# Performance work log

Hardware: AMD Instinct MI355X
Metric: run time of the kernel (lower is better)

## Reference

```python
import jax, jax.numpy as jnp
import numpy as np

# Model constants (match init_kwargs)
H = 256          # hidden_dim
NH = 4           # num_heads
L = 4            # gnn_layers
T = 4            # transformer_layers
KMAX = 10        # k_max for overlap embedding
MAXD = 32        # MAX_DIST
INC = 119        # in_channels (atom vocab)
ED = 5           # edge_dim (bond vocab)
B = 64           # graphs per batch
M_SUB = 32       # subgraphs per graph (m)
KNODE = 32       # nodes per subgraph (k)
S = B * M_SUB    # total subgraphs = 2048
N = S * KNODE    # flattened nodes = 65536
E = 131072       # intra-subgraph directed edges


def _ln(x, g, b):
    mu = x.mean(-1, keepdims=True)
    var = ((x - mu) ** 2).mean(-1, keepdims=True)
    return (x - mu) * jax.lax.rsqrt(var + 1e-5) * g + b


def setup_inputs() -> dict:
    key = jax.random.key(0)
    ks = iter(jax.random.split(key, 24))
    nk = lambda: next(ks)
    rn = lambda k_, shp: 0.02 * jax.random.normal(k_, shp, dtype=jnp.float32)

    x_ids = jax.random.randint(nk(), (N,), 0, INC)
    edge_ids = jax.random.randint(nk(), (E,), 0, ED)
    # intra-subgraph edges: endpoints stay within each block of KNODE nodes
    eps_per = E // S
    base = jnp.repeat(jnp.arange(S) * KNODE, eps_per)
    src = base + jax.random.randint(nk(), (E,), 0, KNODE)
    dst = base + jax.random.randint(nk(), (E,), 0, KNODE)
    ns = jax.random.randint(nk(), (S, KNODE), 0, 500)
    padm = jax.random.uniform(nk(), (S, KNODE)) < 0.1
    nodes_sampled = jnp.where(padm, -1, ns)
    dist = jax.random.randint(nk(), (N,), 0, MAXD + 1)
    lp = -5.0 * jax.random.uniform(nk(), (S,))

    return {
        'x_ids': x_ids, 'edge_ids': edge_ids, 'src': src, 'dst': dst,
        'nodes_sampled': nodes_sampled, 'dist': dist, 'lp': lp,
        'atom_emb': rn(nk(), (INC, H)), 'bond_emb': rn(nk(), (ED, H)),
        'dist_emb': rn(nk(), (MAXD + 1, H)),
        'logp_W': rn(nk(), (H,)), 'logp_b': jnp.zeros((H,)),
        'gnn_eps': jnp.zeros((L,)),
        'gnn_W1': rn(nk(), (L, H, H)), 'gnn_b1': jnp.zeros((L, H)),
        'gnn_W2': rn(nk(), (L, H, H)), 'gnn_b2': jnp.zeros((L, H)),
        'ln1_g': jnp.ones((T, H)), 'ln1_b': jnp.zeros((T, H)),
        'qkv_W': rn(nk(), (T, H, 3 * H)),
        'out_W': rn(nk(), (T, H, H)), 'out_b': jnp.zeros((T, H)),
        'ln2_g': jnp.ones((T, H)), 'ln2_b': jnp.zeros((T, H)),
        'f1_W': rn(nk(), (T, H, 4 * H)), 'f1_b': jnp.zeros((T, 4 * H)),
        'f2_W': rn(nk(), (T, 4 * H, H)), 'f2_b': jnp.zeros((T, H)),
        'lnout_g': jnp.ones((H,)), 'lnout_b': jnp.zeros((H,)),
        'overlap_emb': rn(nk(), (KMAX + 1,)),
        'ht_alpha': jnp.ones(()),
    }


def reference(x_ids, edge_ids, src, dst, nodes_sampled, dist, lp,
              atom_emb, bond_emb, dist_emb, logp_W, logp_b,
              gnn_eps, gnn_W1, gnn_b1, gnn_W2, gnn_b2,
              ln1_g, ln1_b, qkv_W, out_W, out_b, ln2_g, ln2_b,
              f1_W, f1_b, f2_W, f2_b, lnout_g, lnout_b,
              overlap_emb, ht_alpha):
    # ---- flatten / embed node features ----
    valid = (nodes_sampled >= 0).reshape(N)
    valid_f = valid.astype(jnp.float32)[:, None]
    lp = jnp.where(jnp.isfinite(lp), lp, 0.0)
    sub_batch = jnp.arange(N) // KNODE
    dist_c = jnp.clip(dist, 0, MAXD)
    logp_pe = jax.nn.relu(lp[sub_batch][:, None] * logp_W + logp_b)
    h = (atom_emb[x_ids] + dist_emb[dist_c] + logp_pe) * valid_f  # [N,H]
    e = bond_emb[edge_ids]                                        # [E,H]

    # ---- GINE message passing ----
    for l in range(L):
        msg = jax.nn.relu(h[src] + e)                       # [E,H] gather
        agg = jax.ops.segment_sum(msg, dst, num_segments=N) # [N,H] scatter-add
        z = (1.0 + gnn_eps[l]) * h + agg
        z = jax.nn.relu(z @ gnn_W1[l] + gnn_b1[l])
        h = (z @ gnn_W2[l] + gnn_b2[l]) * valid_f

    # ---- pool roots into [B, m, H] tokens ----
    root = jnp.arange(S) * KNODE
    x = h[root].reshape(B, M_SUB, H)
    lp2 = lp.reshape(B, M_SUB)

    # ---- pairwise subgraph overlap bias ----
    nodes = nodes_sampled.reshape(B, M_SUB, KNODE)
    vmask = nodes >= 0
    # eq[b,i,j,ki,kj]: node ki of subgraph i equals node kj of subgraph j
    eq = nodes[:, :, None, :, None] == nodes[:, None, :, None, :]
    overlap = (eq.any(-1) & vmask[:, :, None, :]).sum(-1)  # [B,m,m]
    lp_c = jnp.clip(lp2, -30.0, 0.0)
    bias = overlap_emb[jnp.clip(overlap, 0, KMAX)] - ht_alpha * lp_c[:, None, :]
    bias = bias[:, None]  # [B,1,m,m], broadcast over heads

    # ---- relative-bias transformer ----
    hd = H // NH
    scale = 1.0 / np.sqrt(hd).astype(np.float32)
    for t in range(T):
        r = _ln(x, ln1_g[t], ln1_b[t])
        q, k_, v = jnp.split(r @ qkv_W[t], 3, axis=-1)
        q = q.reshape(B, M_SUB, NH, hd)
        k_ = k_.reshape(B, M_SUB, NH, hd)
        v = v.reshape(B, M_SUB, NH, hd)
        scores = jnp.einsum('bihd,bjhd->bhij', q, k_) * scale + bias
        attn = jax.nn.softmax(scores, axis=-1)
        o = jnp.einsum('bhij,bjhd->bihd', attn, v).reshape(B, M_SUB, H)
        x = x + o @ out_W[t] + out_b[t]
        r2 = _ln(x, ln2_g[t], ln2_b[t])
        x = x + jax.nn.gelu(r2 @ f1_W[t] + f1_b[t], approximate=False) @ f2_W[t] + f2_b[t]

    x = _ln(x, lnout_g, lnout_b)
    # HT-weighted mean over subgraph tokens
    w = jax.nn.softmax(-lp_c, axis=1)
    return (w[:, :, None] * x).sum(1)  # [B,H]
```

## Files before the change

kernel.cpp:

```cpp
#include <hip/hip_runtime.h>
#include <hip/hip_bf16.h>
#include <math.h>

#define HDIM   256
#define NHEAD  4
#define LLAY   4
#define TLAY   4
#define KMAXC  10
#define MAXD   32
#define BATCH  64
#define MSUB   32
#define KNODE  32
#define SSUB   2048
#define NNODE  65536
#define NEDGE  131072
#define EPSPER 64
#define EDN    5

typedef unsigned short u16;
typedef __attribute__((ext_vector_type(8))) short bf16x8;
typedef __attribute__((ext_vector_type(4))) float f32x4;

__device__ __forceinline__ float us2f(u16 u) {
    union { unsigned int i; float f; } x; x.i = ((unsigned int)u) << 16; return x.f;
}
__device__ __forceinline__ u16 f2us(float v) {
    union { float f; unsigned int i; } x; x.f = v;
    unsigned int u = x.i;
    u += 0x7fffu + ((u >> 16) & 1u);
    return (u16)(u >> 16);
}
__device__ __forceinline__ float finite_or_zero(float v) {
    return (v == v && fabsf(v) <= 3.0e38f) ? v : 0.0f;
}
__device__ __forceinline__ void gll16(const u16* g, u16* l) {
    __builtin_amdgcn_global_load_lds(
        (const __attribute__((address_space(1))) unsigned int*)g,
        (__attribute__((address_space(3))) unsigned int*)l, 16, 0, 0);
}

__global__ __launch_bounds__(256) void k_csr(
    const int* __restrict__ src, const int* __restrict__ dst,
    const int* __restrict__ eid, u16* __restrict__ perm, u16* __restrict__ off)
{
    __shared__ int sL[4][64], dL[4][64], eL[4][64];
    int wave = threadIdx.x >> 6, lane = threadIdx.x & 63;
    int sgi = blockIdx.x * 4 + wave;
    sL[wave][lane] = src[sgi * 64 + lane] - sgi * KNODE;
    dL[wave][lane] = dst[sgi * 64 + lane] - sgi * KNODE;
    eL[wave][lane] = eid[sgi * 64 + lane];
    __syncthreads();
    if (lane < 32) {
        int cnt = 0;
        for (int e = 0; e < 64; ++e) cnt += (dL[wave][e] == lane) ? 1 : 0;
        int incl = cnt;
        #pragma unroll
        for (int d = 1; d < 32; d <<= 1) {
            int v = __shfl_up(incl, d, 64);
            if (lane >= d) incl += v;
        }
        int start = incl - cnt;
        off[sgi * 32 + lane] = (u16)start;
        int pos = start;
        for (int e = 0; e < 64; ++e) {
            if (dL[wave][e] == lane) {
                perm[sgi * 64 + pos] = (u16)((sL[wave][e] << 3) | eL[wave][e]);
                ++pos;
            }
        }
    }
}

__global__ __launch_bounds__(256) void k_wtrans(
    const float* __restrict__ W, u16* __restrict__ WT, int K, int N)
{
    __shared__ float til[32][33];
    int k0 = blockIdx.x * 32, n0 = blockIdx.y * 32, s = blockIdx.z;
    const float* Wb = W + (size_t)s * K * N;
    u16* Tb = WT + (size_t)s * N * K;
    int j = threadIdx.x & 31, i0 = threadIdx.x >> 5;
    #pragma unroll
    for (int it = 0; it < 4; ++it) {
        int i = i0 + it * 8;
        til[i][j] = Wb[(size_t)(k0 + i) * N + n0 + j];
    }
    __syncthreads();
    #pragma unroll
    for (int it = 0; it < 4; ++it) {
        int i = i0 + it * 8;
        Tb[(size_t)(n0 + i) * K + k0 + j] = f2us(til[j][i]);
    }
}

__global__ __launch_bounds__(256, 3) void k_gnn4(
    const int* __restrict__ x_ids, const int* __restrict__ dist,
    const int* __restrict__ nodes, const float* __restrict__ lp,
    const float* __restrict__ atom_emb, const float* __restrict__ dist_emb,
    const float* __restrict__ logp_W, const float* __restrict__ logp_b,
    const u16* __restrict__ perm, const u16* __restrict__ off,
    const float* __restrict__ bond_emb, const float* __restrict__ eps_arr,
    const float* __restrict__ b1a, const float* __restrict__ b2a,
    const u16* __restrict__ W1T, const u16* __restrict__ W2T,
    float* __restrict__ x)
{
    __shared__ __align__(16) unsigned char smem[38912];
    u16*   hz    = (u16*)smem;
    float* bondL = (float*)(smem + 32768);
    u16*   permL = (u16*)(smem + 32768 + 5120);
    u16*   offL  = (u16*)(smem + 32768 + 5120 + 256);
    float* validL= (float*)(smem + 32768 + 5120 + 512);
    float* epsL  = (float*)(smem + 32768 + 5120 + 512 + 256);

    int tid = threadIdx.x, lane = tid & 63, wave = tid >> 6;
    int row0 = blockIdx.x * 64;
    int fr = lane & 15, quad = lane >> 4;

    for (int i = tid; i < EDN * 256; i += 256) bondL[i] = bond_emb[i];
    if (tid < 128) permL[tid] = perm[blockIdx.x * 128 + tid];
    if (tid < 64) {
        offL[tid] = off[blockIdx.x * 64 + tid];
        validL[tid] = (nodes[row0 + tid] >= 0) ? 1.0f : 0.0f;
    }
    if (tid < 4) epsL[tid] = eps_arr[tid];

    {
        int m = tid & 63, qd = tid >> 6;
        int rg = row0 + m;
        float valid = (nodes[rg] >= 0) ? 1.0f : 0.0f;
        float lpv = finite_or_zero(lp[rg >> 5]);
        int dc = dist[rg]; dc = dc < 0 ? 0 : (dc > MAXD ? MAXD : dc);
        int xid = x_ids[rg];
        #pragma unroll
        for (int k = 0; k < 8; ++k) {
            int cc = qd * 8 + k, c = cc * 8;
            float4 a0 = *reinterpret_cast<const float4*>(atom_emb + xid * 256 + c);
            float4 a1 = *reinterpret_cast<const float4*>(atom_emb + xid * 256 + c + 4);
            float4 d0 = *reinterpret_cast<const float4*>(dist_emb + dc * 256 + c);
            float4 d1 = *reinterpret_cast<const float4*>(dist_emb + dc * 256 + c + 4);
            float4 w0 = *reinterpret_cast<const float4*>(logp_W + c);
            float4 w1 = *reinterpret_cast<const float4*>(logp_W + c + 4);
            float4 p0 = *reinterpret_cast<const float4*>(logp_b + c);
            float4 p1 = *reinterpret_cast<const float4*>(logp_b + c + 4);
            union { bf16x8 v; ushort4 h[2]; } o;
            o.h[0] = (ushort4){
                f2us((a0.x + d0.x + fmaxf(lpv * w0.x + p0.x, 0.f)) * valid),
                f2us((a0.y + d0.y + fmaxf(lpv * w0.y + p0.y, 0.f)) * valid),
                f2us((a0.z + d0.z + fmaxf(lpv * w0.z + p0.z, 0.f)) * valid),
                f2us((a0.w + d0.w + fmaxf(lpv * w0.w + p0.w, 0.f)) * valid) };
            o.h[1] = (ushort4){
                f2us((a1.x + d1.x + fmaxf(lpv * w1.x + p1.x, 0.f)) * valid),
                f2us((a1.y + d1.y + fmaxf(lpv * w1.y + p1.y, 0.f)) * valid),
                f2us((a1.z + d1.z + fmaxf(lpv * w1.z + p1.z, 0.f)) * valid),
                f2us((a1.w + d1.w + fmaxf(lpv * w1.w + p1.w, 0.f)) * valid) };
            *reinterpret_cast<bf16x8*>(hz + m * 256 + ((cc ^ (m & 7)) * 8)) = o.v;
        }
    }
    __syncthreads();

    int rl = tid >> 3, g8 = tid & 7;
    for (int l = 0; l < LLAY; ++l) {
        float ep1 = 1.0f + epsL[l];
        for (int p = 0; p < 2; ++p) {
            int row = p * 32 + rl;
            int e0 = offL[p * 32 + rl];
            int e1 = (rl < 31) ? offL[p * 32 + rl + 1] : 64;
            float a[32];
            #pragma unroll
            for (int q = 0; q < 32; ++q) a[q] = 0.f;
            for (int j = e0; j < e1; ++j) {
                int ent = permL[p * 64 + j];
                int sl = p * 32 + (ent >> 3);
                int be = ent & 7;
                #pragma unroll
                for (int q = 0; q < 4; ++q) {
                    union { bf16x8 v; u16 s[8]; } hv;
                    hv.v = *reinterpret_cast<const bf16x8*>(
                        hz + sl * 256 + (((g8 * 4 + q) ^ (sl & 7)) * 8));
                    const float* bp = bondL + be * 256 + g8 * 32 + q * 8;
                    float4 bo0 = *reinterpret_cast<const float4*>(bp);
                    float4 bo1 = *reinterpret_cast<const float4*>(bp + 4);
                    a[q*8+0] += fmaxf(us2f(hv.s[0]) + bo0.x, 0.f);
                    a[q*8+1] += fmaxf(us2f(hv.s[1]) + bo0.y, 0.f);
                    a[q*8+2] += fmaxf(us2f(hv.s[2]) + bo0.z, 0.f);
                    a[q*8+3] += fmaxf(us2f(hv.s[3]) + bo0.w, 0.f);
                    a[q*8+4] += fmaxf(us2f(hv.s[4]) + bo1.x, 0.f);
                    a[q*8+5] += fmaxf(us2f(hv.s[5]) + bo1.y, 0.f);
                    a[q*8+6] += fmaxf(us2f(hv.s[6]) + bo1.z, 0.f);
                    a[q*8+7] += fmaxf(us2f(hv.s[7]) + bo1.w, 0.f);
                }
            }
            __syncthreads();
            #pragma unroll
            for (int q = 0; q < 4; ++q) {
                u16* ptr = hz + row * 256 + (((g8 * 4 + q) ^ (row & 7)) * 8);
                union { bf16x8 v; u16 s[8]; } hv, ov;
                hv.v = *reinterpret_cast<const bf16x8*>(ptr);
                #pragma unroll
                for (int k = 0; k < 8; ++k)
                    ov.s[k] = f2us(ep1 * us2f(hv.s[k]) + a[q * 8 + k]);
                *reinterpret_cast<bf16x8*>(ptr) = ov.v;
            }
        }
        __syncthreads();

        const u16* W1 = W1T + l * 65536;
        const float* b1 = b1a + l * 256;
        bf16x8 wf[4][8];
        #pragma unroll
        for (int i = 0; i < 4; ++i)
            #pragma unroll
            for (int kc = 0; kc < 8; ++kc)
                wf[i][kc] = *reinterpret_cast<const bf16x8*>(
                    W1 + (size_t)(wave * 64 + i * 16 + fr) * 256 + kc * 32 + quad * 8);
        f32x4 acc[4][4];
        #pragma unroll
        for (int i = 0; i < 4; ++i)
            #pragma unroll
            for (int j = 0; j < 4; ++j) acc[i][j] = (f32x4){0.f, 0.f, 0.f, 0.f};
        #pragma unroll
        for (int kc = 0; kc < 8; ++kc) {
            bf16x8 bfv[4];
            #pragma unroll
            for (int j = 0; j < 4; ++j) {
                int m = j * 16 + fr;
                bfv[j] = *reinterpret_cast<const bf16x8*>(hz + m * 256 + (((kc * 4 + quad) ^ (m & 7)) * 8));
            }
            #pragma unroll
            for (int i = 0; i < 4; ++i)
                #pragma unroll
                for (int j = 0; j < 4; ++j)
                    acc[i][j] = __builtin_amdgcn_mfma_f32_16x16x32_bf16(wf[i][kc], bfv[j], acc[i][j], 0, 0, 0);
        }
        __syncthreads();
        #pragma unroll
        for (int i = 0; i < 4; ++i) {
            int n1b = wave * 64 + i * 16 + quad * 4;
            float4 bb = *reinterpret_cast<const float4*>(b1 + n1b);
            #pragma unroll
            for (int j = 0; j < 4; ++j) {
                int m = j * 16 + fr;
                ushort4 o = { f2us(fmaxf(acc[i][j][0] + bb.x, 0.f)),
                              f2us(fmaxf(acc[i][j][1] + bb.y, 0.f)),
                              f2us(fmaxf(acc[i][j][2] + bb.z, 0.f)),
                              f2us(fmaxf(acc[i][j][3] + bb.w, 0.f)) };
                *reinterpret_cast<ushort4*>(hz + m * 256 + (((n1b >> 3) ^ (m & 7)) * 8) + (n1b & 7)) = o;
            }
        }
        __syncthreads();

        const u16* W2 = W2T + l * 65536;
        const float* b2 = b2a + l * 256;
        #pragma unroll
        for (int i = 0; i < 4; ++i)
            #pragma unroll
            for (int kc = 0; kc < 8; ++kc)
                wf[i][kc] = *reinterpret_cast<const bf16x8*>(
                    W2 + (size_t)(wave * 64 + i * 16 + fr) * 256 + kc * 32 + quad * 8);
        #pragma unroll
        for (int i = 0; i < 4; ++i)
            #pragma unroll
            for (int j = 0; j < 4; ++j) acc[i][j] = (f32x4){0.f, 0.f, 0.f, 0.f};
        #pragma unroll
        for (int kc = 0; kc < 8; ++kc) {
            bf16x8 bfv[4];
            #pragma unroll
            for (int j = 0; j < 4; ++j) {
                int m = j * 16 + fr;
                bfv[j] = *reinterpret_cast<const bf16x8*>(hz + m * 256 + (((kc * 4 + quad) ^ (m & 7)) * 8));
            }
            #pragma unroll
            for (int i = 0; i < 4; ++i)
                #pragma unroll
                for (int j = 0; j < 4; ++j)
                    acc[i][j] = __builtin_amdgcn_mfma_f32_16x16x32_bf16(wf[i][kc], bfv[j], acc[i][j], 0, 0, 0);
        }
        __syncthreads();

        if (l < LLAY - 1) {
            #pragma unroll
            for (int i = 0; i < 4; ++i) {
                int n2b = wave * 64 + i * 16 + quad * 4;
                float4 bb = *reinterpret_cast<const float4*>(b2 + n2b);
                #pragma unroll
                for (int j = 0; j < 4; ++j) {
                    int m = j * 16 + fr;
                    float vm = validL[m];
                    ushort4 o = { f2us((acc[i][j][0] + bb.x) * vm),
                                  f2us((acc[i][j][1] + bb.y) * vm),
                                  f2us((acc[i][j][2] + bb.z) * vm),
                                  f2us((acc[i][j][3] + bb.w) * vm) };
                    *reinterpret_cast<ushort4*>(hz + m * 256 + (((n2b >> 3) ^ (m & 7)) * 8) + (n2b & 7)) = o;
                }
            }
            __syncthreads();
        } else {
            if (fr == 0) {
                #pragma unroll
                for (int i = 0; i < 4; ++i) {
                    int n2b = wave * 64 + i * 16 + quad * 4;
                    float4 bb = *reinterpret_cast<const float4*>(b2 + n2b);
                    #pragma unroll
                    for (int jj = 0; jj < 2; ++jj) {
                        int j = jj * 2, m = j * 16;
                        float vm = validL[m];
                        float4 o = { (acc[i][j][0] + bb.x) * vm,
                                     (acc[i][j][1] + bb.y) * vm,
                                     (acc[i][j][2] + bb.z) * vm,
                                     (acc[i][j][3] + bb.w) * vm };
                        *reinterpret_cast<float4*>(
                            x + (size_t)(blockIdx.x * 2 + (m >> 5)) * 256 + n2b) = o;
                    }
                }
            }
        }
    }
}

__global__ __launch_bounds__(1024) void k_bias(
    const int* __restrict__ nodes, const float* __restrict__ lp,
    const float* __restrict__ ovl_emb, const float* __restrict__ alpha_p,
    float* __restrict__ bias)
{
    int b = blockIdx.x, tid = threadIdx.x;
    __shared__ int nd[32][32];
    __shared__ unsigned int bmv[32][17];
    __shared__ float lpc[32];
    __shared__ float emb[16];
    nd[tid >> 5][tid & 31] = nodes[b * 1024 + tid];
    if (tid < 512) bmv[tid >> 4][tid & 15] = 0u;
    if (tid < 32) {
        float l = finite_or_zero(lp[b * 32 + tid]);
        l = l < -30.f ? -30.f : (l > 0.f ? 0.f : l);
        lpc[tid] = l;
    }
    if (tid >= 64 && tid < 64 + KMAXC + 1) emb[tid - 64] = ovl_emb[tid - 64];
    __syncthreads();
    int own = nd[tid >> 5][tid & 31];
    if (own >= 0) atomicOr(&bmv[tid >> 5][own >> 5], 1u << (own & 31));
    __syncthreads();
    int i = tid >> 5, j = tid & 31;
    float alpha = alpha_p[0];
    int cnt = 0;
    #pragma unroll
    for (int k = 0; k < 32; ++k) {
        int nk = nd[i][k];
        if (nk >= 0) cnt += (int)((bmv[j][nk >> 5] >> (nk & 31)) & 1u);
    }
    bias[b * 1024 + tid] = emb[cnt > KMAXC ? KMAXC : cnt] - alpha * lpc[j];
}

__global__ __launch_bounds__(256) void k_gemmA_ln(
    const float* __restrict__ X, const u16* __restrict__ BT,
    const float* __restrict__ ln_g, const float* __restrict__ ln_b,
    const float* __restrict__ bias, u16* __restrict__ C,
    int N, int act)
{
    __shared__ __align__(16) u16 As[64 * 256];
    __shared__ __align__(16) u16 Bs[2][64 * 32];
    int tid = threadIdx.x, lane = tid & 63, wave = tid >> 6;
    int wm = wave >> 1, wn = wave & 1;
    int bm = blockIdx.y * 64, bn = blockIdx.x * 64;
    int fr = lane & 15, quad = lane >> 4;

    const u16* gB = BT + (size_t)(bn + wave * 16 + (lane >> 2)) * 256 + (lane & 3) * 8;
    gll16(gB, &Bs[0][wave * 512]);

    #pragma unroll
    for (int rr = 0; rr < 16; ++rr) {
        int r = wave * 16 + rr;
        float4 xv = *reinterpret_cast<const float4*>(X + (size_t)(bm + r) * 256 + lane * 4);
        float s = xv.x + xv.y + xv.z + xv.w;
        #pragma unroll
        for (int o2 = 32; o2 > 0; o2 >>= 1) s += __shfl_xor(s, o2);
        float mu = s * (1.0f / 256.0f);
        float d0 = xv.x - mu, d1 = xv.y - mu, d2 = xv.z - mu, d3 = xv.w - mu;
        float sq = d0 * d0 + d1 * d1 + d2 * d2 + d3 * d3;
        #pragma unroll
        for (int o2 = 32; o2 > 0; o2 >>= 1) sq += __shfl_xor(sq, o2);
        float rs = rsqrtf(sq * (1.0f / 256.0f) + 1e-5f);
        int c = lane * 4;
        float4 gv = *reinterpret_cast<const float4*>(ln_g + c);
        float4 bv = *reinterpret_cast<const float4*>(ln_b + c);
        ushort4 o = { f2us(d0 * rs * gv.x + bv.x), f2us(d1 * rs * gv.y + bv.y),
                      f2us(d2 * rs * gv.z + bv.z), f2us(d3 * rs * gv.w + bv.w) };
        *reinterpret_cast<ushort4*>(As + r * 256 + (((lane >> 1) ^ (r & 7)) * 8) + (lane & 1) * 4) = o;
    }
    __syncthreads();

    f32x4 acc[2][2];
    #pragma unroll
    for (int i = 0; i < 2; ++i)
        #pragma unroll
        for (int j = 0; j < 2; ++j) acc[i][j] = (f32x4){0.f, 0.f, 0.f, 0.f};
    for (int kc = 0; kc < 8; ++kc) {
        int buf = kc & 1;
        if (kc < 7) gll16(gB + (kc + 1) * 32, &Bs[buf ^ 1][wave * 512]);
        bf16x8 af[2], bfr[2];
        #pragma unroll
        for (int i = 0; i < 2; ++i) {
            int m = wm * 32 + i * 16 + fr;
            af[i] = *reinterpret_cast<const bf16x8*>(As + m * 256 + (((kc * 4 + quad) ^ (m & 7)) * 8));
        }
        #pragma unroll
        for (int j = 0; j < 2; ++j)
            bfr[j] = *reinterpret_cast<const bf16x8*>(&Bs[buf][(wn * 32 + j * 16 + fr) * 32 + quad * 8]);
        #pragma unroll
        for (int i = 0; i < 2; ++i)
            #pragma unroll
            for (int j = 0; j < 2; ++j)
                acc[i][j] = __builtin_amdgcn_mfma_f32_16x16x32_bf16(af[i], bfr[j], acc[i][j], 0, 0, 0);
        __syncthreads();
    }
    int crow0 = bm + wm * 32 + quad * 4;
    int ccol0 = bn + wn * 32 + fr;
    #pragma unroll
    for (int i = 0; i < 2; ++i) {
        #pragma unroll
        for (int r = 0; r < 4; ++r) {
            int m = crow0 + i * 16 + r;
            #pragma unroll
            for (int j = 0; j < 2; ++j) {
                int n = ccol0 + j * 16;
                float v = acc[i][j][r];
                if (bias) v += bias[n];
                if (act == 2) v = 0.5f * v * (1.0f + erff(v * 0.70710678118654752f));
                C[(size_t)m * N + n] = f2us(v);
            }
        }
    }
}

__global__ __launch_bounds__(256) void k_gemmB(
    const u16* __restrict__ A, const u16* __restrict__ BT,
    const float* __restrict__ bias, void* __restrict__ Cout, int c_is_bf16,
    const float* __restrict__ resid, const int* __restrict__ valid,
    int M, int K, int N, int act)
{
    __shared__ __align__(16) u16 As[2][64 * 32];
    __shared__ __align__(16) u16 Bs[2][64 * 32];
    int tid = threadIdx.x, lane = tid & 63, wave = tid >> 6;
    int wm = wave >> 1, wn = wave & 1;
    int bm = blockIdx.y * 64, bn = blockIdx.x * 64;
    const u16* gA = A + (size_t)(bm + wave * 16 + (lane >> 2)) * K + (lane & 3) * 8;
    const u16* gB = BT + (size_t)(bn + wave * 16 + (lane >> 2)) * K + (lane & 3) * 8;
    gll16(gA, &As[0][wave * 512]);
    gll16(gB, &Bs[0][wave * 512]);
    f32x4 acc[2][2];
    #pragma unroll
    for (int i = 0; i < 2; ++i)
        #pragma unroll
        for (int j = 0; j < 2; ++j) acc[i][j] = (f32x4){0.f, 0.f, 0.f, 0.f};
    int fr = lane & 15, quad = lane >> 4;
    int nit = K >> 5;
    __syncthreads();
    for (int it = 0; it < nit; ++it) {
        int buf = it & 1;
        if (it + 1 < nit) {
            int k0 = (it + 1) * 32;
            gll16(gA + k0, &As[buf ^ 1][wave * 512]);
            gll16(gB + k0, &Bs[buf ^ 1][wave * 512]);
        }
        bf16x8 af[2], bfr[2];
        #pragma unroll
        for (int i = 0; i < 2; ++i)
            af[i] = *reinterpret_cast<const bf16x8*>(&As[buf][(wm * 32 + i * 16 + fr) * 32 + quad * 8]);
        #pragma unroll
        for (int j = 0; j < 2; ++j)
            bfr[j] = *reinterpret_cast<const bf16x8*>(&Bs[buf][(wn * 32 + j * 16 + fr) * 32 + quad * 8]);
        #pragma unroll
        for (int i = 0; i < 2; ++i)
            #pragma unroll
            for (int j = 0; j < 2; ++j)
                acc[i][j] = __builtin_amdgcn_mfma_f32_16x16x32_bf16(af[i], bfr[j], acc[i][j], 0, 0, 0);
        __syncthreads();
    }
    int crow0 = bm + wm * 32 + quad * 4;
    int ccol0 = bn + wn * 32 + fr;
    #pragma unroll
    for (int i = 0; i < 2; ++i) {
        #pragma unroll
        for (int r = 0; r < 4; ++r) {
            int m = crow0 + i * 16 + r;
            float vm = valid ? ((valid[m] >= 0) ? 1.0f : 0.0f) : 1.0f;
            #pragma unroll
            for (int j = 0; j < 2; ++j) {
                int n = ccol0 + j * 16;
                float v = acc[i][j][r];
                if (bias) v += bias[n];
                if (act == 1) v = v > 0.f ? v : 0.f;
                else if (act == 2) v = 0.5f * v * (1.0f + erff(v * 0.70710678118654752f));
                v *= vm;
                if (resid) v += resid[(size_t)m * N + n];
                if (c_is_bf16) ((u16*)Cout)[(size_t)m * N + n] = f2us(v);
                else ((float*)Cout)[(size_t)m * N + n] = v;
            }
        }
    }
}

__global__ __launch_bounds__(256) void k_attn(
    const u16* __restrict__ qkv, const float* __restrict__ bias, u16* __restrict__ o)
{
    int b = blockIdx.x >> 2, hh = blockIdx.x & 3;
    __shared__ float qs[32][65], ks[32][65], vs[32][65];
    __shared__ float sc[32][33];
    int tid = threadIdx.x;
    #pragma unroll
    for (int u = 0; u < 8; ++u) {
        int idx = tid + u * 256;
        int i = idx >> 6, d = idx & 63;
        size_t base = (size_t)(b * 32 + i) * 768;
        qs[i][d] = us2f(qkv[base + hh * 64 + d]);
        ks[i][d] = us2f(qkv[base + 256 + hh * 64 + d]);
        vs[i][d] = us2f(qkv[base + 512 + hh * 64 + d]);
    }
    __syncthreads();
    #pragma unroll
    for (int u = 0; u < 4; ++u) {
        int p = tid + u * 256;
        int i = p >> 5, j = p & 31;
        float s = 0.f;
        #pragma unroll
        for (int d = 0; d < 64; ++d) s += qs[i][d] * ks[j][d];
        sc[i][j] = s * 0.125f + bias[b * 1024 + i * 32 + j];
    }
    __syncthreads();
    if (tid < 32) {
        int i = tid;
        float m = -1e30f;
        for (int j = 0; j < 32; ++j) m = fmaxf(m, sc[i][j]);
        float sum = 0.f;
        for (int j = 0; j < 32; ++j) { float e = expf(sc[i][j] - m); sc[i][j] = e; sum += e; }
        float inv = 1.0f / sum;
        for (int j = 0; j < 32; ++j) sc[i][j] *= inv;
    }
    __syncthreads();
    #pragma unroll
    for (int u = 0; u < 8; ++u) {
        int idx = tid + u * 256;
        int i = idx >> 6, d = idx & 63;
        float a = 0.f;
        #pragma unroll
        for (int j = 0; j < 32; ++j) a += sc[i][j] * vs[j][d];
        o[(size_t)(b * 32 + i) * 256 + hh * 64 + d] = f2us(a);
    }
}

__global__ __launch_bounds__(256) void k_fin(
    const float* __restrict__ x, const float* __restrict__ lp,
    const float* __restrict__ lnout_g, const float* __restrict__ lnout_b,
    float* __restrict__ out)
{
    __shared__ __align__(16) float xlnf[32 * 260];
    __shared__ float wfin[32];
    int tid = threadIdx.x, lane = tid & 63, wave = tid >> 6;
    int b = blockIdx.x;
    #pragma unroll
    for (int rr = 0; rr < 8; ++rr) {
        int row = wave * 8 + rr;
        float4 xv = *reinterpret_cast<const float4*>(x + (size_t)(b * 32 + row) * 256 + lane * 4);
        float s = xv.x + xv.y + xv.z + xv.w;
        #pragma unroll
        for (int o2 = 32; o2 > 0; o2 >>= 1) s += __shfl_xor(s, o2);
        float mu = s * (1.0f / 256.0f);
        float d0 = xv.x - mu, d1 = xv.y - mu, d2 = xv.z - mu, d3 = xv.w - mu;
        float sq = d0 * d0 + d1 * d1 + d2 * d2 + d3 * d3;
        #pragma unroll
        for (int o2 = 32; o2 > 0; o2 >>= 1) sq += __shfl_xor(sq, o2);
        float rs = rsqrtf(sq * (1.0f / 256.0f) + 1e-5f);
        int c = lane * 4;
        float4 gv = *reinterpret_cast<const float4*>(lnout_g + c);
        float4 bv = *reinterpret_cast<const float4*>(lnout_b + c);
        float4 o = { d0 * rs * gv.x + bv.x, d1 * rs * gv.y + bv.y,
                     d2 * rs * gv.z + bv.z, d3 * rs * gv.w + bv.w };
        *reinterpret_cast<float4*>(xlnf + row * 260 + c) = o;
    }
    __syncthreads();
    if (tid == 0) {
        float l2[32];
        float m = -1e30f;
        for (int i = 0; i < 32; ++i) {
            float l = finite_or_zero(lp[b * 32 + i]);
            l = l < -30.f ? -30.f : (l > 0.f ? 0.f : l);
            l2[i] = -l;
            m = fmaxf(m, -l);
        }
        float s = 0.f;
        for (int i = 0; i < 32; ++i) { float e = expf(l2[i] - m); wfin[i] = e; s += e; }
        float inv = 1.0f / s;
        for (int i = 0; i < 32; ++i) wfin[i] *= inv;
    }
    __syncthreads();
    float a = 0.f;
    for (int i = 0; i < 32; ++i) a += wfin[i] * xlnf[i * 260 + tid];
    out[(size_t)b * 256 + tid] = a;
}

extern "C" void kernel_launch(void* const* d_in, const int* in_sizes, int n_in,
                              void* d_out, int out_size, void* d_ws, size_t ws_size,
                              hipStream_t stream)
{
    const int*   x_ids    = (const int*)d_in[0];
    const int*   edge_ids = (const int*)d_in[1];
    const int*   srcp     = (const int*)d_in[2];
    const int*   dstp     = (const int*)d_in[3];
    const int*   nodes    = (const int*)d_in[4];
    const int*   dist     = (const int*)d_in[5];
    const float* lp       = (const float*)d_in[6];
    const float* atom_emb = (const float*)d_in[7];
    const float* bond_emb = (const float*)d_in[8];
    const float* dist_emb = (const float*)d_in[9];
    const float* logp_W   = (const float*)d_in[10];
    const float* logp_b   = (const float*)d_in[11];
    const float* gnn_eps  = (const float*)d_in[12];
    const float* gnn_W1   = (const float*)d_in[13];
    const float* gnn_b1   = (const float*)d_in[14];
    const float* gnn_W2   = (const float*)d_in[15];
    const float* gnn_b2   = (const float*)d_in[16];
    const float* ln1_g    = (const float*)d_in[17];
    const float* ln1_b    = (const float*)d_in[18];
    const float* qkv_W    = (const float*)d_in[19];
    const float* out_W    = (const float*)d_in[20];
    const float* out_b    = (const float*)d_in[21];
    const float* ln2_g    = (const float*)d_in[22];
    const float* ln2_b    = (const float*)d_in[23];
    const float* f1_W     = (const float*)d_in[24];
    const float* f1_b     = (const float*)d_in[25];
    const float* f2_W     = (const float*)d_in[26];
    const float* f2_b     = (const float*)d_in[27];
    const float* lnout_g  = (const float*)d_in[28];
    const float* lnout_b  = (const float*)d_in[29];
    const float* ovl_emb  = (const float*)d_in[30];
    const float* alpha    = (const float*)d_in[31];

    char* ws = (char*)d_ws;
    u16*   gW1T  = (u16*)(ws + 100663296ull);
    u16*   gW2T  = (u16*)(ws + 100663296ull + 524288ull);
    u16*   permW = (u16*)(ws + 100663296ull + 1048576ull);
    u16*   offW  = (u16*)(ws + 100663296ull + 1310720ull);
    u16*   qkvT  = (u16*)(ws + 33554432ull);
    u16*   outT  = (u16*)(ws + 33554432ull + 1572864ull);
    u16*   f1T   = (u16*)(ws + 33554432ull + 2097152ull);
    u16*   f2T   = (u16*)(ws + 33554432ull + 4194304ull);
    u16*   ob    = (u16*)(ws + 33554432ull + 6291456ull);
    float* biasb = (float*)(ws + 33554432ull + 7340032ull);
    u16*   qkvb  = (u16*)(ws + 33554432ull + 7602176ull);
    u16*   ffh   = (u16*)(ws + 33554432ull + 10747904ull);
    float* x     = (float*)(ws + 67108864ull);

    k_csr<<<SSUB / 4, 256, 0, stream>>>(srcp, dstp, edge_ids, permW, offW);
    k_wtrans<<<dim3(8, 8, 4), 256, 0, stream>>>(gnn_W1, gW1T, 256, 256);
    k_wtrans<<<dim3(8, 8, 4), 256, 0, stream>>>(gnn_W2, gW2T, 256, 256);
    k_gnn4<<<NNODE / 64, 256, 0, stream>>>(
        x_ids, dist, nodes, lp, atom_emb, dist_emb, logp_W, logp_b,
        permW, offW, bond_emb, gnn_eps, gnn_b1, gnn_b2, gW1T, gW2T, x);
    k_wtrans<<<dim3(8, 24, 4), 256, 0, stream>>>(qkv_W, qkvT, 256, 768);
    k_wtrans<<<dim3(8, 8, 4), 256, 0, stream>>>(out_W, outT, 256, 256);
    k_wtrans<<<dim3(8, 32, 4), 256, 0, stream>>>(f1_W, f1T, 256, 1024);
    k_wtrans<<<dim3(32, 8, 4), 256, 0, stream>>>(f2_W, f2T, 1024, 256);
    k_bias<<<BATCH, 1024, 0, stream>>>(nodes, lp, ovl_emb, alpha, biasb);
    for (int t = 0; t < TLAY; ++t) {
        k_gemmA_ln<<<dim3(12, 32), 256, 0, stream>>>(
            x, qkvT + (size_t)t * 768 * 256, ln1_g + t * 256, ln1_b + t * 256,
            nullptr, qkvb, 768, 0);
        k_attn<<<BATCH * NHEAD, 256, 0, stream>>>(qkvb, biasb, ob);
        k_gemmB<<<dim3(4, 32), 256, 0, stream>>>(
            ob, outT + (size_t)t * 65536, out_b + t * 256, x, 0,
            x, nullptr, SSUB, 256, 256, 0);
        k_gemmA_ln<<<dim3(16, 32), 256, 0, stream>>>(
            x, f1T + (size_t)t * 1024 * 256, ln2_g + t * 256, ln2_b + t * 256,
            f1_b + t * 1024, ffh, 1024, 2);
        k_gemmB<<<dim3(4, 32), 256, 0, stream>>>(
            ffh, f2T + (size_t)t * 256 * 1024, f2_b + t * 256, x, 0,
            x, nullptr, SSUB, 1024, 256, 0);
    }
    k_fin<<<BATCH, 256, 0, stream>>>(x, lp, lnout_g, lnout_b, (float*)d_out);
}
```

Before: 608.0 us.

## Shrink GNN and transformer GEMM tiles to 32 rows and swizzle LDS

The GNN kernel now processes one 32-node subgraph per block instead of two, which halves LDS use and launches twice as many blocks. Weight fragments are loaded from global memory inside the k-loop instead of being held in registers, which cuts register pressure at the cost of repeated weight reads. The transformer GEMMs move to 32-row tiles with XOR-swizzled LDS layouts to avoid bank conflicts, and gemmB is specialized for its fp32 residual epilogue. The goal is more occupancy and parallelism on small matrices, traded against more weight traffic and less MFMA work per block.

Result: no change. 614.0 us (+1.0%).

```diff
diff --git a/kernel.cpp b/kernel.cpp
--- a/kernel.cpp
+++ b/kernel.cpp
@@ -16,6 +16,7 @@
 #define NEDGE  131072
 #define EPSPER 64
 #define EDN    5
+#define BSTR   264
 
 typedef unsigned short u16;
 typedef __attribute__((ext_vector_type(8))) short bf16x8;
@@ -103,36 +104,39 @@
     const u16* __restrict__ W1T, const u16* __restrict__ W2T,
     float* __restrict__ x)
 {
-    __shared__ __align__(16) unsigned char smem[38912];
+    __shared__ __align__(16) unsigned char smem[22144];
     u16*   hz    = (u16*)smem;
-    float* bondL = (float*)(smem + 32768);
-    u16*   permL = (u16*)(smem + 32768 + 5120);
-    u16*   offL  = (u16*)(smem + 32768 + 5120 + 256);
-    float* validL= (float*)(smem + 32768 + 5120 + 512);
-    float* epsL  = (float*)(smem + 32768 + 5120 + 512 + 256);
+    float* bondL = (float*)(smem + 16384);
+    u16*   permL = (u16*)(smem + 21760);
+    u16*   offL  = (u16*)(smem + 21888);
+    float* validL= (float*)(smem + 21952);
+    float* epsL  = (float*)(smem + 22080);
 
     int tid = threadIdx.x, lane = tid & 63, wave = tid >> 6;
-    int row0 = blockIdx.x * 64;
+    int sg = blockIdx.x, row0 = sg * 32;
     int fr = lane & 15, quad = lane >> 4;
 
-    for (int i = tid; i < EDN * 256; i += 256) bondL[i] = bond_emb[i];
-    if (tid < 128) permL[tid] = perm[blockIdx.x * 128 + tid];
-    if (tid < 64) {
-        offL[tid] = off[blockIdx.x * 64 + tid];
+    for (int i = tid; i < EDN * BSTR; i += 256) {
+        int r = i / BSTR, c = i - r * BSTR;
+        bondL[i] = (c < 256) ? bond_emb[r * 256 + c] : 0.f;
+    }
+    if (tid < 64) permL[tid] = perm[sg * 64 + tid];
+    if (tid < 32) {
+        offL[tid] = off[sg * 32 + tid];
         validL[tid] = (nodes[row0 + tid] >= 0) ? 1.0f : 0.0f;
     }
     if (tid < 4) epsL[tid] = eps_arr[tid];
 
     {
-        int m = tid & 63, qd = tid >> 6;
+        int m = tid >> 3, t8 = tid & 7;
         int rg = row0 + m;
         float valid = (nodes[rg] >= 0) ? 1.0f : 0.0f;
         float lpv = finite_or_zero(lp[rg >> 5]);
         int dc = dist[rg]; dc = dc < 0 ? 0 : (dc > MAXD ? MAXD : dc);
         int xid = x_ids[rg];
         #pragma unroll
-        for (int k = 0; k < 8; ++k) {
-            int cc = qd * 8 + k, c = cc * 8;
+        for (int k = 0; k < 4; ++k) {
+            int cc = t8 * 4 + k, c = cc * 8;
             float4 a0 = *reinterpret_cast<const float4*>(atom_emb + xid * 256 + c);
             float4 a1 = *reinterpret_cast<const float4*>(atom_emb + xid * 256 + c + 4);
             float4 d0 = *reinterpret_cast<const float4*>(dist_emb + dc * 256 + c);
@@ -160,23 +164,22 @@
     int rl = tid >> 3, g8 = tid & 7;
     for (int l = 0; l < LLAY; ++l) {
         float ep1 = 1.0f + epsL[l];
-        for (int p = 0; p < 2; ++p) {
-            int row = p * 32 + rl;
-            int e0 = offL[p * 32 + rl];
-            int e1 = (rl < 31) ? offL[p * 32 + rl + 1] : 64;
+        {
+            int e0 = offL[rl];
+            int e1 = (rl < 31) ? offL[rl + 1] : 64;
             float a[32];
             #pragma unroll
             for (int q = 0; q < 32; ++q) a[q] = 0.f;
             for (int j = e0; j < e1; ++j) {
-                int ent = permL[p * 64 + j];
-                int sl = p * 32 + (ent >> 3);
-                int be = ent & 7;
+                int ent = permL[j];
+                int sl = ent >> 3, be = ent & 7;
                 #pragma unroll
                 for (int q = 0; q < 4; ++q) {
+                    int cc = q * 8 + g8;
                     union { bf16x8 v; u16 s[8]; } hv;
                     hv.v = *reinterpret_cast<const bf16x8*>(
-                        hz + sl * 256 + (((g8 * 4 + q) ^ (sl & 7)) * 8));
-                    const float* bp = bondL + be * 256 + g8 * 32 + q * 8;
+                        hz + sl * 256 + ((cc ^ (sl & 7)) * 8));
+                    const float* bp = bondL + be * BSTR + cc * 8;
                     float4 bo0 = *reinterpret_cast<const float4*>(bp);
                     float4 bo1 = *reinterpret_cast<const float4*>(bp + 4);
                     a[q*8+0] += fmaxf(us2f(hv.s[0]) + bo0.x, 0.f);
@@ -192,7 +195,8 @@
             __syncthreads();
             #pragma unroll
             for (int q = 0; q < 4; ++q) {
-                u16* ptr = hz + row * 256 + (((g8 * 4 + q) ^ (row & 7)) * 8);
+                int cc = q * 8 + g8;
+                u16* ptr = hz + rl * 256 + ((cc ^ (rl & 7)) * 8);
                 union { bf16x8 v; u16 s[8]; } hv, ov;
                 hv.v = *reinterpret_cast<const bf16x8*>(ptr);
                 #pragma unroll
@@ -205,31 +209,24 @@
 
         const u16* W1 = W1T + l * 65536;
         const float* b1 = b1a + l * 256;
-        bf16x8 wf[4][8];
-        #pragma unroll
-        for (int i = 0; i < 4; ++i)
-            #pragma unroll
-            for (int kc = 0; kc < 8; ++kc)
-                wf[i][kc] = *reinterpret_cast<const bf16x8*>(
-                    W1 + (size_t)(wave * 64 + i * 16 + fr) * 256 + kc * 32 + quad * 8);
-        f32x4 acc[4][4];
-        #pragma unroll
-        for (int i = 0; i < 4; ++i)
-            #pragma unroll
-            for (int j = 0; j < 4; ++j) acc[i][j] = (f32x4){0.f, 0.f, 0.f, 0.f};
+        f32x4 acc[4][2];
+        #pragma unroll
+        for (int i = 0; i < 4; ++i) { acc[i][0] = (f32x4){0,0,0,0}; acc[i][1] = (f32x4){0,0,0,0}; }
         #pragma unroll
         for (int kc = 0; kc < 8; ++kc) {
-            bf16x8 bfv[4];
-            #pragma unroll
-            for (int j = 0; j < 4; ++j) {
+            bf16x8 bfv[2];
+            #pragma unroll
+            for (int j = 0; j < 2; ++j) {
                 int m = j * 16 + fr;
                 bfv[j] = *reinterpret_cast<const bf16x8*>(hz + m * 256 + (((kc * 4 + quad) ^ (m & 7)) * 8));
             }
             #pragma unroll
-            for (int i = 0; i < 4; ++i)
-                #pragma unroll
-                for (int j = 0; j < 4; ++j)
-                    acc[i][j] = __builtin_amdgcn_mfma_f32_16x16x32_bf16(wf[i][kc], bfv[j], acc[i][j], 0, 0, 0);
+            for (int i = 0; i < 4; ++i) {
+                bf16x8 wf = *reinterpret_cast<const bf16x8*>(
+                    W1 + (size_t)(wave * 64 + i * 16 + fr) * 256 + kc * 32 + quad * 8);
+                acc[i][0] = __builtin_amdgcn_mfma_f32_16x16x32_bf16(wf, bfv[0], acc[i][0], 0, 0, 0);
+                acc[i][1] = __builtin_amdgcn_mfma_f32_16x16x32_bf16(wf, bfv[1], acc[i][1], 0, 0, 0);
+            }
         }
         __syncthreads();
         #pragma unroll
@@ -237,7 +234,7 @@
             int n1b = wave * 64 + i * 16 + quad * 4;
             float4 bb = *reinterpret_cast<const float4*>(b1 + n1b);
             #pragma unroll
-            for (int j = 0; j < 4; ++j) {
+            for (int j = 0; j < 2; ++j) {
                 int m = j * 16 + fr;
                 ushort4 o = { f2us(fmaxf(acc[i][j][0] + bb.x, 0.f)),
                               f2us(fmaxf(acc[i][j][1] + bb.y, 0.f)),
@@ -251,38 +248,31 @@
         const u16* W2 = W2T + l * 65536;
         const float* b2 = b2a + l * 256;
         #pragma unroll
-        for (int i = 0; i < 4; ++i)
-            #pragma unroll
-            for (int kc = 0; kc < 8; ++kc)
-                wf[i][kc] = *reinterpret_cast<const bf16x8*>(
-                    W2 + (size_t)(wave * 64 + i * 16 + fr) * 256 + kc * 32 + quad * 8);
-        #pragma unroll
-        for (int i = 0; i < 4; ++i)
-            #pragma unroll
-            for (int j = 0; j < 4; ++j) acc[i][j] = (f32x4){0.f, 0.f, 0.f, 0.f};
+        for (int i = 0; i < 4; ++i) { acc[i][0] = (f32x4){0,0,0,0}; acc[i][1] = (f32x4){0,0,0,0}; }
         #pragma unroll
         for (int kc = 0; kc < 8; ++kc) {
-            bf16x8 bfv[4];
-            #pragma unroll
-            for (int j = 0; j < 4; ++j) {
+            bf16x8 bfv[2];
+            #pragma unroll
+            for (int j = 0; j < 2; ++j) {
                 int m = j * 16 + fr;
                 bfv[j] = *reinterpret_cast<const bf16x8*>(hz + m * 256 + (((kc * 4 + quad) ^ (m & 7)) * 8));
             }
             #pragma unroll
-            for (int i = 0; i < 4; ++i)
-                #pragma unroll
-                for (int j = 0; j < 4; ++j)
-                    acc[i][j] = __builtin_amdgcn_mfma_f32_16x16x32_bf16(wf[i][kc], bfv[j], acc[i][j], 0, 0, 0);
+            for (int i = 0; i < 4; ++i) {
+                bf16x8 wf = *reinterpret_cast<const bf16x8*>(
+                    W2 + (size_t)(wave * 64 + i * 16 + fr) * 256 + kc * 32 + quad * 8);
+                acc[i][0] = __builtin_amdgcn_mfma_f32_16x16x32_bf16(wf, bfv[0], acc[i][0], 0, 0, 0);
+                acc[i][1] = __builtin_amdgcn_mfma_f32_16x16x32_bf16(wf, bfv[1], acc[i][1], 0, 0, 0);
+            }
         }
         __syncthreads();
-
         if (l < LLAY - 1) {
             #pragma unroll
             for (int i = 0; i < 4; ++i) {
                 int n2b = wave * 64 + i * 16 + quad * 4;
                 float4 bb = *reinterpret_cast<const float4*>(b2 + n2b);
                 #pragma unroll
-                for (int j = 0; j < 4; ++j) {
+                for (int j = 0; j < 2; ++j) {
                     int m = j * 16 + fr;
                     float vm = validL[m];
                     ushort4 o = { f2us((acc[i][j][0] + bb.x) * vm),
@@ -295,21 +285,14 @@
             __syncthreads();
         } else {
             if (fr == 0) {
+                float vm = validL[0];
                 #pragma unroll
                 for (int i = 0; i < 4; ++i) {
                     int n2b = wave * 64 + i * 16 + quad * 4;
                     float4 bb = *reinterpret_cast<const float4*>(b2 + n2b);
-                    #pragma unroll
-                    for (int jj = 0; jj < 2; ++jj) {
-                        int j = jj * 2, m = j * 16;
-                        float vm = validL[m];
-                        float4 o = { (acc[i][j][0] + bb.x) * vm,
-                                     (acc[i][j][1] + bb.y) * vm,
-                                     (acc[i][j][2] + bb.z) * vm,
-                                     (acc[i][j][3] + bb.w) * vm };
-                        *reinterpret_cast<float4*>(
-                            x + (size_t)(blockIdx.x * 2 + (m >> 5)) * 256 + n2b) = o;
-                    }
+                    float4 o = { (acc[i][0][0] + bb.x) * vm, (acc[i][0][1] + bb.y) * vm,
+                                 (acc[i][0][2] + bb.z) * vm, (acc[i][0][3] + bb.w) * vm };
+                    *reinterpret_cast<float4*>(x + (size_t)sg * 256 + n2b) = o;
                 }
             }
         }
@@ -355,19 +338,21 @@
     const float* __restrict__ bias, u16* __restrict__ C,
     int N, int act)
 {
-    __shared__ __align__(16) u16 As[64 * 256];
+    __shared__ __align__(16) u16 As[32 * 256];
     __shared__ __align__(16) u16 Bs[2][64 * 32];
     int tid = threadIdx.x, lane = tid & 63, wave = tid >> 6;
     int wm = wave >> 1, wn = wave & 1;
-    int bm = blockIdx.y * 64, bn = blockIdx.x * 64;
+    int bm = blockIdx.y * 32, bn = blockIdx.x * 64;
     int fr = lane & 15, quad = lane >> 4;
 
-    const u16* gB = BT + (size_t)(bn + wave * 16 + (lane >> 2)) * 256 + (lane & 3) * 8;
+    int srow = lane >> 2, skq = lane & 3;
+    const u16* gB = BT + (size_t)(bn + wave * 16 + srow) * 256
+                       + (skq ^ ((srow >> 1) & 3)) * 8;
     gll16(gB, &Bs[0][wave * 512]);
 
     #pragma unroll
-    for (int rr = 0; rr < 16; ++rr) {
-        int r = wave * 16 + rr;
+    for (int rr = 0; rr < 8; ++rr) {
+        int r = wave * 8 + rr;
         float4 xv = *reinterpret_cast<const float4*>(X + (size_t)(bm + r) * 256 + lane * 4);
         float s = xv.x + xv.y + xv.z + xv.w;
         #pragma unroll
@@ -387,113 +372,93 @@
     }
     __syncthreads();
 
-    f32x4 acc[2][2];
-    #pragma unroll
-    for (int i = 0; i < 2; ++i)
-        #pragma unroll
-        for (int j = 0; j < 2; ++j) acc[i][j] = (f32x4){0.f, 0.f, 0.f, 0.f};
+    f32x4 acc[2];
+    acc[0] = (f32x4){0,0,0,0}; acc[1] = (f32x4){0,0,0,0};
     for (int kc = 0; kc < 8; ++kc) {
         int buf = kc & 1;
         if (kc < 7) gll16(gB + (kc + 1) * 32, &Bs[buf ^ 1][wave * 512]);
-        bf16x8 af[2], bfr[2];
-        #pragma unroll
-        for (int i = 0; i < 2; ++i) {
-            int m = wm * 32 + i * 16 + fr;
-            af[i] = *reinterpret_cast<const bf16x8*>(As + m * 256 + (((kc * 4 + quad) ^ (m & 7)) * 8));
-        }
-        #pragma unroll
-        for (int j = 0; j < 2; ++j)
-            bfr[j] = *reinterpret_cast<const bf16x8*>(&Bs[buf][(wn * 32 + j * 16 + fr) * 32 + quad * 8]);
-        #pragma unroll
-        for (int i = 0; i < 2; ++i)
-            #pragma unroll
-            for (int j = 0; j < 2; ++j)
-                acc[i][j] = __builtin_amdgcn_mfma_f32_16x16x32_bf16(af[i], bfr[j], acc[i][j], 0, 0, 0);
+        int am = wm * 16 + fr;
+        bf16x8 af = *reinterpret_cast<const bf16x8*>(
+            As + am * 256 + (((kc * 4 + quad) ^ (am & 7)) * 8));
+        bf16x8 bfr[2];
+        #pragma unroll
+        for (int j = 0; j < 2; ++j) {
+            int br = wn * 32 + j * 16 + fr;
+            bfr[j] = *reinterpret_cast<const bf16x8*>(
+                &Bs[buf][br * 32 + (quad ^ ((br >> 1) & 3)) * 8]);
+        }
+        acc[0] = __builtin_amdgcn_mfma_f32_16x16x32_bf16(af, bfr[0], acc[0], 0, 0, 0);
+        acc[1] = __builtin_amdgcn_mfma_f32_16x16x32_bf16(af, bfr[1], acc[1], 0, 0, 0);
         __syncthreads();
     }
-    int crow0 = bm + wm * 32 + quad * 4;
+    int crow0 = bm + wm * 16 + quad * 4;
     int ccol0 = bn + wn * 32 + fr;
     #pragma unroll
-    for (int i = 0; i < 2; ++i) {
-        #pragma unroll
-        for (int r = 0; r < 4; ++r) {
-            int m = crow0 + i * 16 + r;
-            #pragma unroll
-            for (int j = 0; j < 2; ++j) {
-                int n = ccol0 + j * 16;
-                float v = acc[i][j][r];
-                if (bias) v += bias[n];
-                if (act == 2) v = 0.5f * v * (1.0f + erff(v * 0.70710678118654752f));
-                C[(size_t)m * N + n] = f2us(v);
-            }
+    for (int r = 0; r < 4; ++r) {
+        int m = crow0 + r;
+        #pragma unroll
+        for (int j = 0; j < 2; ++j) {
+            int n = ccol0 + j * 16;
+            float v = acc[j][r];
+            if (bias) v += bias[n];
+            if (act == 2) v = 0.5f * v * (1.0f + erff(v * 0.70710678118654752f));
+            C[(size_t)m * N + n] = f2us(v);
         }
     }
 }
 
 __global__ __launch_bounds__(256) void k_gemmB(
     const u16* __restrict__ A, const u16* __restrict__ BT,
-    const float* __restrict__ bias, void* __restrict__ Cout, int c_is_bf16,
-    const float* __restrict__ resid, const int* __restrict__ valid,
-    int M, int K, int N, int act)
-{
-    __shared__ __align__(16) u16 As[2][64 * 32];
+    const float* __restrict__ bias, float* __restrict__ Cout,
+    const float* __restrict__ resid, int M, int K, int N)
+{
+    __shared__ __align__(16) u16 As[2][32 * 32];
     __shared__ __align__(16) u16 Bs[2][64 * 32];
     int tid = threadIdx.x, lane = tid & 63, wave = tid >> 6;
     int wm = wave >> 1, wn = wave & 1;
-    int bm = blockIdx.y * 64, bn = blockIdx.x * 64;
-    const u16* gA = A + (size_t)(bm + wave * 16 + (lane >> 2)) * K + (lane & 3) * 8;
-    const u16* gB = BT + (size_t)(bn + wave * 16 + (lane >> 2)) * K + (lane & 3) * 8;
-    gll16(gA, &As[0][wave * 512]);
+    int bm = blockIdx.y * 32, bn = blockIdx.x * 64;
+    int fr = lane & 15, quad = lane >> 4;
+    int srow = lane >> 2, skq = lane & 3;
+    int koff = (skq ^ ((srow >> 1) & 3)) * 8;
+    const u16* gA = A + (size_t)(bm + (wave & 1) * 16 + srow) * K + koff;
+    const u16* gB = BT + (size_t)(bn + wave * 16 + srow) * K + koff;
+    if (wave < 2) gll16(gA, &As[0][wave * 512]);
     gll16(gB, &Bs[0][wave * 512]);
-    f32x4 acc[2][2];
-    #pragma unroll
-    for (int i = 0; i < 2; ++i)
-        #pragma unroll
-        for (int j = 0; j < 2; ++j) acc[i][j] = (f32x4){0.f, 0.f, 0.f, 0.f};
-    int fr = lane & 15, quad = lane >> 4;
+    f32x4 acc[2];
+    acc[0] = (f32x4){0,0,0,0}; acc[1] = (f32x4){0,0,0,0};
     int nit = K >> 5;
     __syncthreads();
     for (int it = 0; it < nit; ++it) {
         int buf = it & 1;
         if (it + 1 < nit) {
             int k0 = (it + 1) * 32;
-            gll16(gA + k0, &As[buf ^ 1][wave * 512]);
+            if (wave < 2) gll16(gA + k0, &As[buf ^ 1][wave * 512]);
             gll16(gB + k0, &Bs[buf ^ 1][wave * 512]);
         }
-        bf16x8 af[2], bfr[2];
-        #pragma unroll
-        for (int i = 0; i < 2; ++i)
-            af[i] = *reinterpret_cast<const bf16x8*>(&As[buf][(wm * 32 + i * 16 + fr) * 32 + quad * 8]);
-        #pragma unroll
-        for (int j = 0; j < 2; ++j)
-            bfr[j] = *reinterpret_cast<const bf16x8*>(&Bs[buf][(wn * 32 + j * 16 + fr) * 32 + quad * 8]);
-        #pragma unroll
-        for (int i = 0; i < 2; ++i)
-            #pragma unroll
-            for (int j = 0; j < 2; ++j)
-                acc[i][j] = __builtin_amdgcn_mfma_f32_16x16x32_bf16(af[i], bfr[j], acc[i][j], 0, 0, 0);
+        int am = wm * 16 + fr;
+        bf16x8 af = *reinterpret_cast<const bf16x8*>(
+            &As[buf][am * 32 + (quad ^ ((am >> 1) & 3)) * 8]);
+        bf16x8 bfr[2];
+        #pragma unroll
+        for (int j = 0; j < 2; ++j) {
+            int br = wn * 32 + j * 16 + fr;
+            bfr[j] = *reinterpret_cast<const bf16x8*>(
+                &Bs[buf][br * 32 + (quad ^ ((br >> 1) & 3)) * 8]);
+        }
+        acc[0] = __builtin_amdgcn_mfma_f32_16x16x32_bf16(af, bfr[0], acc[0], 0, 0, 0);
+        acc[1] = __builtin_amdgcn_mfma_f32_16x16x32_bf16(af, bfr[1], acc[1], 0, 0, 0);
         __syncthreads();
     }
-    int crow0 = bm + wm * 32 + quad * 4;
+    int crow0 = bm + wm * 16 + quad * 4;
     int ccol0 = bn + wn * 32 + fr;
     #pragma unroll
-    for (int i = 0; i < 2; ++i) {
-        #pragma unroll
-        for (int r = 0; r < 4; ++r) {
-            int m = crow0 + i * 16 + r;
-            float vm = valid ? ((valid[m] >= 0) ? 1.0f : 0.0f) : 1.0f;
-            #pragma unroll
-            for (int j = 0; j < 2; ++j) {
-                int n = ccol0 + j * 16;
-                float v = acc[i][j][r];
-                if (bias) v += bias[n];
-                if (act == 1) v = v > 0.f ? v : 0.f;
-                else if (act == 2) v = 0.5f * v * (1.0f + erff(v * 0.70710678118654752f));
-                v *= vm;
-                if (resid) v += resid[(size_t)m * N + n];
-                if (c_is_bf16) ((u16*)Cout)[(size_t)m * N + n] = f2us(v);
-                else ((float*)Cout)[(size_t)m * N + n] = v;
-            }
+    for (int r = 0; r < 4; ++r) {
+        int m = crow0 + r;
+        #pragma unroll
+        for (int j = 0; j < 2; ++j) {
+            int n = ccol0 + j * 16;
+            float v = acc[j][r] + bias[n] + resid[(size_t)m * N + n];
+            Cout[(size_t)m * N + n] = v;
         }
     }
 }
@@ -651,7 +616,7 @@
     k_csr<<<SSUB / 4, 256, 0, stream>>>(srcp, dstp, edge_ids, permW, offW);
     k_wtrans<<<dim3(8, 8, 4), 256, 0, stream>>>(gnn_W1, gW1T, 256, 256);
     k_wtrans<<<dim3(8, 8, 4), 256, 0, stream>>>(gnn_W2, gW2T, 256, 256);
-    k_gnn4<<<NNODE / 64, 256, 0, stream>>>(
+    k_gnn4<<<SSUB, 256, 0, stream>>>(
         x_ids, dist, nodes, lp, atom_emb, dist_emb, logp_W, logp_b,
         permW, offW, bond_emb, gnn_eps, gnn_b1, gnn_b2, gW1T, gW2T, x);
     k_wtrans<<<dim3(8, 24, 4), 256, 0, stream>>>(qkv_W, qkvT, 256, 768);
@@ -660,19 +625,17 @@
     k_wtrans<<<dim3(32, 8, 4), 256, 0, stream>>>(f2_W, f2T, 1024, 256);
     k_bias<<<BATCH, 1024, 0, stream>>>(nodes, lp, ovl_emb, alpha, biasb);
     for (int t = 0; t < TLAY; ++t) {
-        k_gemmA_ln<<<dim3(12, 32), 256, 0, stream>>>(
+        k_gemmA_ln<<<dim3(12, 64), 256, 0, stream>>>(
             x, qkvT + (size_t)t * 768 * 256, ln1_g + t * 256, ln1_b + t * 256,
             nullptr, qkvb, 768, 0);
         k_attn<<<BATCH * NHEAD, 256, 0, stream>>>(qkvb, biasb, ob);
-        k_gemmB<<<dim3(4, 32), 256, 0, stream>>>(
-            ob, outT + (size_t)t * 65536, out_b + t * 256, x, 0,
-            x, nullptr, SSUB, 256, 256, 0);
-        k_gemmA_ln<<<dim3(16, 32), 256, 0, stream>>>(
+        k_gemmB<<<dim3(4, 64), 256, 0, stream>>>(
+            ob, outT + (size_t)t * 65536, out_b + t * 256, x, x, SSUB, 256, 256);
+        k_gemmA_ln<<<dim3(16, 64), 256, 0, stream>>>(
             x, f1T + (size_t)t * 1024 * 256, ln2_g + t * 256, ln2_b + t * 256,
             f1_b + t * 1024, ffh, 1024, 2);
-        k_gemmB<<<dim3(4, 32), 256, 0, stream>>>(
-            ffh, f2T + (size_t)t * 256 * 1024, f2_b + t * 256, x, 0,
-            x, nullptr, SSUB, 1024, 256, 0);
+        k_gemmB<<<dim3(4, 64), 256, 0, stream>>>(
+            ffh, f2T + (size_t)t * 256 * 1024, f2_b + t * 256, x, x, SSUB, 1024, 256);
     }
     k_fin<<<BATCH, 256, 0, stream>>>(x, lp, lnout_g, lnout_b, (float*)d_out);
 }
```
